# Kernel tuning notes

Hardware: AMD Instinct MI355X
Metric: run time of the kernel (lower is better)

The kernel has to match this reference:

```python
import jax, jax.numpy as jnp
import numpy as np

B, S, D, H = 2, 2048, 1024, 16  # batch, seq, rep_dim, num_heads
DH = D // H
MASK_VALUE = -1e-06  # value passed by MHAttention to masked_softmax (NOT -1e6)


def setup_inputs() -> dict:
    key = jax.random.key(0)
    ks = jax.random.split(key, 16)
    def xavier(k, shape):
        fan_in, fan_out = shape[0], shape[1]
        limit = float(np.sqrt(6.0 / (fan_in + fan_out)))
        return jax.random.uniform(k, shape, jnp.float32, -limit, limit)
    return {
        "queries": jax.random.normal(ks[0], (B, S, D), jnp.float32),
        "keys": jax.random.normal(ks[1], (B, S, D), jnp.float32),
        "values": jax.random.normal(ks[2], (B, S, D), jnp.float32),
        "thresholds": jax.random.randint(ks[3], (B,), 1, S + 1, jnp.int32),
        # Linear params stored as (in, out) so y = x @ W + b
        "Wq": xavier(ks[4], (D, D)), "bq": jnp.zeros((D,), jnp.float32),
        "Wk": xavier(ks[5], (D, D)), "bk": jnp.zeros((D,), jnp.float32),
        "Wv": xavier(ks[6], (D, D)), "bv": jnp.zeros((D,), jnp.float32),
        "W": xavier(ks[7], (DH, DH)),  # learnable bilinear attention matrix
        "Wo": xavier(ks[8], (D, D)), "bo": jnp.zeros((D,), jnp.float32),
    }


def reference(queries, keys, values, thresholds, Wq, bq, Wk, bk, Wv, bv, W, Wo, bo):
    def split_heads(x):  # (B,S,D) -> (B,H,S,DH)
        return x.reshape(B, S, H, DH).transpose(0, 2, 1, 3)

    Q = split_heads(queries @ Wq + bq)
    K = split_heads(keys @ Wk + bk)
    V = split_heads(values @ Wv + bv)

    # bilinear scores: (Q @ W) @ K^T, no 1/sqrt(d) scaling in original
    scores = jnp.einsum("bhqd,bhkd->bhqk", Q @ W, K)
    # mask key positions >= threshold[b] with MASK_VALUE before softmax
    keep = jnp.arange(S)[None, None, None, :] < thresholds[:, None, None, None]
    scores = jnp.where(keep, scores, MASK_VALUE)
    attn = jax.nn.softmax(scores, axis=-1)

    out = jnp.einsum("bhqk,bhkd->bhqd", attn, V)
    out = out.transpose(0, 2, 1, 3).reshape(B, S, D)  # merge heads
    return out @ Wo + bo
```

## Files before the change

kernel.cpp:

```cpp
#include <hip/hip_runtime.h>
#include <hip/hip_bf16.h>

#define D_MODEL 1024
#define NHEADS  16
#define DH      64
#define SEQ     2048
#define BATCH   2

#define LOG2E 1.4426950408889634f
#define MASKB2 (-1e-6f * LOG2E)
#define DEFER_THR 11.5456f
#define NEG_INF (-__builtin_inff())

typedef __attribute__((ext_vector_type(8))) short short8;
typedef __attribute__((ext_vector_type(4))) short short4v;
typedef __attribute__((ext_vector_type(4))) float f32x4;

#define AS1C(p) ((const __attribute__((address_space(1))) void*)(p))
#define AS3(p)  ((__attribute__((address_space(3))) void*)(p))

union PB { short4v s4; unsigned int u[2]; };
union VU { short8 s8; short4v h[2]; };

static __device__ __forceinline__ float fexp2(float x) {
    return __builtin_amdgcn_exp2f(x);
}

static __device__ __forceinline__ unsigned int pk2(float lo, float hi) {
    __hip_bfloat16 a = __float2bfloat16(lo), b = __float2bfloat16(hi);
    unsigned short au = *(unsigned short*)&a, bu = *(unsigned short*)&b;
    return (unsigned int)au | ((unsigned int)bu << 16);
}

__global__ __launch_bounds__(256) void prep_all_kernel(
    const float* __restrict__ Wq, const float* __restrict__ bq, const float* __restrict__ W,
    __hip_bfloat16* __restrict__ WqT, float* __restrict__ bq2,
    const float* __restrict__ Wk, const float* __restrict__ Wv, const float* __restrict__ Wo,
    __hip_bfloat16* __restrict__ WkT, __hip_bfloat16* __restrict__ WvT,
    __hip_bfloat16* __restrict__ WoT,
    const float* __restrict__ q, const float* __restrict__ k, const float* __restrict__ v,
    __hip_bfloat16* __restrict__ oq, __hip_bfloat16* __restrict__ ok,
    __hip_bfloat16* __restrict__ ov) {
    const int blk = blockIdx.x;
    const int t = threadIdx.x;

    if (blk < 1056) {
        const int c0 = (blk & 31) * 32;
        const int yy = blk >> 5;
        const int h = c0 >> 6, j0 = c0 & 63;
        if (yy == 32) {
            if (t < 32) {
                int col = c0 + t, j = col & 63;
                float s = 0.f;
#pragma unroll
                for (int d = 0; d < DH; ++d) s += bq[h * DH + d] * W[d * DH + j];
                bq2[col] = s * LOG2E;
            }
            return;
        }
        const int r0 = yy * 32;
        __shared__ float sWq[32][68];
        __shared__ float sW[64][36];
        __shared__ float sOut[32][33];
        {
            int lr = t >> 3, lc8 = (t & 7) * 8;
            const float* src = Wq + (size_t)(r0 + lr) * D_MODEL + h * DH + lc8;
            *(float4*)&sWq[lr][lc8]     = *(const float4*)(src);
            *(float4*)&sWq[lr][lc8 + 4] = *(const float4*)(src + 4);
            int d = t >> 2, c8 = (t & 3) * 8;
            const float* wsrc = W + (size_t)d * DH + j0 + c8;
            *(float4*)&sW[d][c8]     = *(const float4*)(wsrc);
            *(float4*)&sW[d][c8 + 4] = *(const float4*)(wsrc + 4);
        }
        __syncthreads();
        {
            int col_loc = t & 31, rq = t >> 5;
            float acc0 = 0.f, acc1 = 0.f, acc2 = 0.f, acc3 = 0.f;
#pragma unroll
            for (int d = 0; d < 64; ++d) {
                float wv = sW[d][col_loc];
                acc0 += sWq[rq * 4 + 0][d] * wv;
                acc1 += sWq[rq * 4 + 1][d] * wv;
                acc2 += sWq[rq * 4 + 2][d] * wv;
                acc3 += sWq[rq * 4 + 3][d] * wv;
            }
            sOut[col_loc][rq * 4 + 0] = acc0 * LOG2E;
            sOut[col_loc][rq * 4 + 1] = acc1 * LOG2E;
            sOut[col_loc][rq * 4 + 2] = acc2 * LOG2E;
            sOut[col_loc][rq * 4 + 3] = acc3 * LOG2E;
        }
        __syncthreads();
        {
            int orow = t >> 3, oc4 = (t & 7) * 4;
            __hip_bfloat16 o4[4];
#pragma unroll
            for (int i = 0; i < 4; ++i) o4[i] = __float2bfloat16(sOut[orow][oc4 + i]);
            *(short4*)(WqT + (size_t)(c0 + orow) * D_MODEL + r0 + oc4) = *(short4*)o4;
        }
    } else if (blk < 4128) {
        __shared__ float sT[32][33];
        int r = blk - 1056;
        int z = r >> 10; r &= 1023;
        const float* Win = (z == 0) ? Wk : (z == 1) ? Wv : Wo;
        __hip_bfloat16* Wt = (z == 0) ? WkT : (z == 1) ? WvT : WoT;
        int n0 = (r & 31) * 32, k0 = (r >> 5) * 32;
        int tx = t & 31, ty = t >> 5;
#pragma unroll
        for (int i = 0; i < 4; ++i)
            sT[ty + i * 8][tx] = Win[(size_t)(k0 + ty + i * 8) * D_MODEL + n0 + tx];
        __syncthreads();
#pragma unroll
        for (int i = 0; i < 4; ++i)
            Wt[(size_t)(n0 + ty + i * 8) * D_MODEL + k0 + tx] =
                __float2bfloat16(sT[tx][ty + i * 8]);
    } else {
        int idx = blk - 4128;
        int z = idx >> 11;
        int i = (idx & 2047) * 256 + t;
        const float* in = (z == 0) ? q : (z == 1) ? k : v;
        __hip_bfloat16* out = (z == 0) ? oq : (z == 1) ? ok : ov;
        float4 a = *(const float4*)(in + (size_t)i * 8);
        float4 b = *(const float4*)(in + (size_t)i * 8 + 4);
        __hip_bfloat16 o[8];
        o[0] = __float2bfloat16(a.x); o[1] = __float2bfloat16(a.y);
        o[2] = __float2bfloat16(a.z); o[3] = __float2bfloat16(a.w);
        o[4] = __float2bfloat16(b.x); o[5] = __float2bfloat16(b.y);
        o[6] = __float2bfloat16(b.z); o[7] = __float2bfloat16(b.w);
        *(short8*)(out + (size_t)i * 8) = *(short8*)o;
    }
}

#define GEMM_CORE(A_, BT_)                                                                  \
    __shared__ __hip_bfloat16 sA[2][128 * 32];                                              \
    __shared__ __hip_bfloat16 sB[2][128 * 32];                                              \
    const int t = threadIdx.x;                                                              \
    const int lane = t & 63, w = t >> 6;                                                    \
    const int g = lane >> 4, li = lane & 15;                                                \
    const int lin = blockIdx.y * 8 + blockIdx.x;                                            \
    const int ob = (lin & 7) * 32 + (lin >> 3);                                             \
    const int r0 = (ob >> 3) * 128, c0 = (ob & 7) * 128;                                    \
    const int wr = (w >> 1) * 64, wc = (w & 1) * 64;                                        \
    f32x4 acc[4][4] = {};                                                                   \
    auto stage = [&](int bb, int k0) {                                                      \
        _Pragma("unroll")                                                                   \
        for (int i = 0; i < 2; ++i) {                                                       \
            int o = (i * 4 + w) * 1024 + lane * 16;                                         \
            int row = o >> 6, ce = (o & 63) >> 1;                                           \
            __builtin_amdgcn_global_load_lds(AS1C(A_ + (size_t)(r0 + row) * 1024 + k0 + ce),\
                                             AS3((char*)sA[bb] + (i * 4 + w) * 1024), 16, 0, 0); \
            __builtin_amdgcn_global_load_lds(AS1C(BT_ + (size_t)(c0 + row) * 1024 + k0 + ce),\
                                             AS3((char*)sB[bb] + (i * 4 + w) * 1024), 16, 0, 0); \
        }                                                                                   \
    };                                                                                      \
    stage(0, 0);                                                                            \
    asm volatile("s_waitcnt vmcnt(0)" ::: "memory");                                        \
    __syncthreads();                                                                        \
    int cur = 0;                                                                            \
    for (int k0 = 0; k0 < 1024; k0 += 32) {                                                 \
        if (k0 + 32 < 1024) stage(cur ^ 1, k0 + 32);                                        \
        short8 af[4], bf[4];                                                                \
        _Pragma("unroll")                                                                   \
        for (int m = 0; m < 4; ++m)                                                         \
            af[m] = *(const short8*)(sA[cur] + (wr + m * 16 + li) * 32 + g * 8);            \
        _Pragma("unroll")                                                                   \
        for (int n = 0; n < 4; ++n)                                                         \
            bf[n] = *(const short8*)(sB[cur] + (wc + n * 16 + li) * 32 + g * 8);            \
        _Pragma("unroll")                                                                   \
        for (int m = 0; m < 4; ++m)                                                         \
            _Pragma("unroll")                                                               \
            for (int n = 0; n < 4; ++n)                                                     \
                acc[m][n] = __builtin_amdgcn_mfma_f32_16x16x32_bf16(af[m], bf[n], acc[m][n], 0, 0, 0); \
        asm volatile("s_waitcnt vmcnt(0)" ::: "memory");                                    \
        __syncthreads();                                                                    \
        cur ^= 1;                                                                           \
    }

__global__ __launch_bounds__(256) void gemm_qkv_kernel(
    const __hip_bfloat16* __restrict__ Xq, const __hip_bfloat16* __restrict__ Xk,
    const __hip_bfloat16* __restrict__ Xv,
    const __hip_bfloat16* __restrict__ WqT, const __hip_bfloat16* __restrict__ WkT,
    const __hip_bfloat16* __restrict__ WvT,
    const float* __restrict__ bq2, const float* __restrict__ bk, const float* __restrict__ bv,
    __hip_bfloat16* __restrict__ Qp, __hip_bfloat16* __restrict__ Kp,
    __hip_bfloat16* __restrict__ Vt) {
    const int z = blockIdx.z;
    const __hip_bfloat16* A  = (z == 0) ? Xq  : (z == 1) ? Xk  : Xv;
    const __hip_bfloat16* BT = (z == 0) ? WqT : (z == 1) ? WkT : WvT;
    const float* bias        = (z == 0) ? bq2 : (z == 1) ? bk  : bv;
    __hip_bfloat16* C        = (z == 0) ? Qp  : (z == 1) ? Kp  : Vt;

    GEMM_CORE(A, BT)

#pragma unroll
    for (int m = 0; m < 4; ++m) {
#pragma unroll
        for (int n = 0; n < 4; ++n) {
            int col = c0 + wc + n * 16 + li;
            float bs = bias[col];
            int row0 = r0 + wr + m * 16 + g * 4;
            int h = col >> 6, d = col & 63;
            if (z == 2) {
                int b = row0 >> 11, s0 = row0 & 2047;
                int sp = (s0 & ~127) | (((s0 >> 2) & 3) << 5) | (((s0 >> 4) & 7) << 2);
                __hip_bfloat16 o4[4];
#pragma unroll
                for (int r = 0; r < 4; ++r) o4[r] = __float2bfloat16(acc[m][n][r] + bs);
                *(short4*)(C + (((size_t)(b * NHEADS + h)) * DH + d) * SEQ + sp) = *(short4*)o4;
            } else {
#pragma unroll
                for (int r = 0; r < 4; ++r) {
                    int row = row0 + r;
                    int b = row >> 11, s = row & 2047;
                    C[(((size_t)(b * NHEADS + h)) * SEQ + s) * DH + d] =
                        __float2bfloat16(acc[m][n][r] + bs);
                }
            }
        }
    }
}

__global__ __launch_bounds__(256) void gemm_out_kernel(
    const __hip_bfloat16* __restrict__ A, const __hip_bfloat16* __restrict__ BT,
    const float* __restrict__ bias, float* __restrict__ C) {
    GEMM_CORE(A, BT)
#pragma unroll
    for (int m = 0; m < 4; ++m) {
#pragma unroll
        for (int n = 0; n < 4; ++n) {
            int col = c0 + wc + n * 16 + li;
            float bs = bias[col];
            int row0 = r0 + wr + m * 16 + g * 4;
#pragma unroll
            for (int r = 0; r < 4; ++r)
                C[(size_t)(row0 + r) * D_MODEL + col] = acc[m][n][r] + bs;
        }
    }
}

__global__ __launch_bounds__(256) void vsum_kernel(const __hip_bfloat16* __restrict__ Vt,
                                                   const int* __restrict__ thresholds,
                                                   float* __restrict__ Vsum) {
    int bh = blockIdx.x, b = bh >> 4;
    int thresh = thresholds[b];
    int loop_end = min(SEQ, ((thresh + 127) >> 7) << 7);
    int t = threadIdx.x;
    int dh = t >> 2, sub = t & 3;
    const __hip_bfloat16* row = Vt + ((size_t)bh * DH + dh) * SEQ;
    float s = 0.f;
    for (int s0 = loop_end + sub * 8; s0 < SEQ; s0 += 32) {
        short8 v = *(const short8*)(row + s0);
#pragma unroll
        for (int j = 0; j < 8; ++j) {
            unsigned short us = (unsigned short)v[j];
            s += __bfloat162float(*(__hip_bfloat16*)&us);
        }
    }
    s += __shfl_xor(s, 1);
    s += __shfl_xor(s, 2);
    if (sub == 0) Vsum[bh * DH + dh] = s;
}

__global__ __launch_bounds__(512, 4) void attn_mfma_kernel(
    const __hip_bfloat16* __restrict__ Qp,
    const __hip_bfloat16* __restrict__ Kp,
    const __hip_bfloat16* __restrict__ Vt,
    const int* __restrict__ thresholds,
    const float* __restrict__ Vsum,
    __hip_bfloat16* __restrict__ AO) {
    __shared__ char lds[65536];
    char* sK  = lds;
    char* sVT = lds + 32768;

    const int t = threadIdx.x, lane = t & 63, w = t >> 6;
    const int g = lane >> 4, li = lane & 15;
    const int bh = blockIdx.x, b = bh >> 4, h = bh & 15;
    const int q0 = blockIdx.y * 128;
    const int thresh = thresholds[b];
    const int loop_end = min(SEQ, ((thresh + 127) >> 7) << 7);
    const __hip_bfloat16* Qb = Qp + (size_t)bh * SEQ * DH;
    const __hip_bfloat16* Kb = Kp + (size_t)bh * SEQ * DH;
    const __hip_bfloat16* Vb = Vt + (size_t)bh * DH * SEQ;

    short8 qf[2];
#pragma unroll
    for (int kb = 0; kb < 2; ++kb)
        qf[kb] = *(const short8*)(Qb + (size_t)(q0 + w * 16 + li) * DH + kb * 32 + g * 8);

    f32x4 Oacc[4] = {};
    float mrun = NEG_INF, lpart = 0.f;

    auto stageK = [&](int bb, int kv) {
#pragma unroll
        for (int i = 0; i < 2; ++i) {
            int o = i * 8192 + t * 16;
            int key = o >> 7, slot = (o & 127) >> 4;
            __builtin_amdgcn_global_load_lds(
                AS1C(Kb + (size_t)(kv + key) * DH + ((slot ^ (key & 7)) << 3)),
                AS3(sK + bb * 16384 + i * 8192 + w * 1024), 16, 0, 0);
        }
    };
    auto stageV = [&](int bb, int kv) {
#pragma unroll
        for (int i = 0; i < 2; ++i) {
            int o = i * 8192 + t * 16;
            int dh = o >> 8, slot = (o & 255) >> 4;
            __builtin_amdgcn_global_load_lds(
                AS1C(Vb + (size_t)dh * SEQ + kv + ((slot ^ (dh & 15)) << 3)),
                AS3(sVT + bb * 16384 + i * 8192 + w * 1024), 16, 0, 0);
        }
    };

    stageK(0, 0); stageV(0, 0);
    asm volatile("s_waitcnt vmcnt(0)" ::: "memory");
    __syncthreads();

    int cur = 0;
    for (int kv0 = 0; kv0 < loop_end; kv0 += 128) {
        int nxt = kv0 + 128;
        if (nxt < loop_end) { stageK(cur ^ 1, nxt); stageV(cur ^ 1, nxt); }

        f32x4 S[8] = {};
        __builtin_amdgcn_s_setprio(1);
#pragma unroll
        for (int kb = 0; kb < 2; ++kb) {
            short8 kf[8];
#pragma unroll
            for (int n = 0; n < 8; ++n) {
                int key = 16 * n + li;
                kf[n] = *(const short8*)(sK + cur * 16384 + key * 128 +
                                         (((4 * kb + g) ^ (key & 7)) << 4));
            }
#pragma unroll
            for (int n = 0; n < 8; ++n)
                S[n] = __builtin_amdgcn_mfma_f32_16x16x32_bf16(kf[n], qf[kb], S[n], 0, 0, 0);
        }
        __builtin_amdgcn_s_setprio(0);

        if (kv0 + 128 > thresh) {
            int tr = thresh - kv0 - 4 * g;
#pragma unroll
            for (int n = 0; n < 8; ++n)
#pragma unroll
                for (int rr = 0; rr < 4; ++rr)
                    if (16 * n + rr >= tr) S[n][rr] = MASKB2;
        }

        float mx = S[0][0];
#pragma unroll
        for (int n = 0; n < 8; ++n)
#pragma unroll
            for (int rr = 0; rr < 4; ++rr) mx = fmaxf(mx, S[n][rr]);
        mx = fmaxf(mx, __shfl_xor(mx, 16));
        mx = fmaxf(mx, __shfl_xor(mx, 32));
        float pmax = mx;

        if (__any(pmax > mrun + DEFER_THR)) {
            float mn = fmaxf(mrun, pmax);
            float alpha = fexp2(mrun - mn);
            lpart *= alpha;
#pragma unroll
            for (int n = 0; n < 4; ++n)
#pragma unroll
                for (int rr = 0; rr < 4; ++rr) Oacc[n][rr] *= alpha;
            mrun = mn;
        }

        short4v pb[8];
#pragma unroll
        for (int n = 0; n < 8; ++n) {
#pragma unroll
            for (int rr = 0; rr < 4; ++rr) {
                float p = fexp2(S[n][rr] - mrun);
                S[n][rr] = p;
                lpart += p;
            }
            PB u;
            u.u[0] = pk2(S[n][0], S[n][1]);
            u.u[1] = pk2(S[n][2], S[n][3]);
            pb[n] = u.s4;
        }

        __builtin_amdgcn_s_setprio(1);
#pragma unroll
        for (int u = 0; u < 4; ++u) {
            int slot = 4 * g + u;
#pragma unroll
            for (int n = 0; n < 4; ++n) {
                int dh = 16 * n + li;
                VU vu;
                vu.s8 = *(const short8*)(sVT + cur * 16384 + dh * 256 +
                                         ((slot ^ (dh & 15)) << 4));
                Oacc[n] = __builtin_amdgcn_mfma_f32_16x16x16bf16_1k(vu.h[0], pb[2 * u],
                                                                    Oacc[n], 0, 0, 0);
                Oacc[n] = __builtin_amdgcn_mfma_f32_16x16x16bf16_1k(vu.h[1], pb[2 * u + 1],
                                                                    Oacc[n], 0, 0, 0);
            }
        }
        __builtin_amdgcn_s_setprio(0);

        asm volatile("s_waitcnt vmcnt(0)" ::: "memory");
        __syncthreads();
        cur ^= 1;
    }

    float lrun = lpart;
    lrun += __shfl_xor(lrun, 16);
    lrun += __shfl_xor(lrun, 32);

    int nmask = SEQ - loop_end;
    if (nmask > 0) {
        const float* vs = Vsum + bh * DH;
        f32x4 vsf[4];
#pragma unroll
        for (int n = 0; n < 4; ++n) vsf[n] = *(const f32x4*)(vs + 16 * n + 4 * g);
        float pu = fexp2(MASKB2 - mrun);
        lrun += (float)nmask * pu;
#pragma unroll
        for (int n = 0; n < 4; ++n)
#pragma unroll
            for (int rr = 0; rr < 4; ++rr) Oacc[n][rr] += pu * vsf[n][rr];
    }

    float linv = 1.0f / lrun;
    int q = q0 + w * 16 + li;
#pragma unroll
    for (int n = 0; n < 4; ++n) {
        __hip_bfloat16 o4[4];
#pragma unroll
        for (int rr = 0; rr < 4; ++rr) o4[rr] = __float2bfloat16(Oacc[n][rr] * linv);
        *(short4*)(AO + (size_t)(b * SEQ + q) * D_MODEL + h * DH + 16 * n + 4 * g) =
            *(short4*)o4;
    }
}

extern "C" void kernel_launch(void* const* d_in, const int* in_sizes, int n_in,
                              void* d_out, int out_size, void* d_ws, size_t ws_size,
                              hipStream_t stream) {
    const float* queries    = (const float*)d_in[0];
    const float* keys       = (const float*)d_in[1];
    const float* values     = (const float*)d_in[2];
    const int*   thresholds = (const int*)d_in[3];
    const float* Wq = (const float*)d_in[4];
    const float* bq = (const float*)d_in[5];
    const float* Wk = (const float*)d_in[6];
    const float* bk = (const float*)d_in[7];
    const float* Wv = (const float*)d_in[8];
    const float* bv = (const float*)d_in[9];
    const float* W  = (const float*)d_in[10];
    const float* Wo = (const float*)d_in[11];
    const float* bo = (const float*)d_in[12];
    float* out = (float*)d_out;

    char* wsb = (char*)d_ws;
    float* bq2  = (float*)wsb;
    float* Vsum = (float*)(wsb + 4096);
    __hip_bfloat16* XqB = (__hip_bfloat16*)(wsb + 16384);
    __hip_bfloat16* XkB = XqB + (1 << 22);
    __hip_bfloat16* XvB = XkB + (1 << 22);
    __hip_bfloat16* WqT = XvB + (1 << 22);
    __hip_bfloat16* WkT = WqT + (1 << 20);
    __hip_bfloat16* WvT = WkT + (1 << 20);
    __hip_bfloat16* WoT = WvT + (1 << 20);
    __hip_bfloat16* QpB = WoT + (1 << 20);
    __hip_bfloat16* KpB = QpB + (1 << 22);
    __hip_bfloat16* VtB = KpB + (1 << 22);
    __hip_bfloat16* AOB = XqB;

    prep_all_kernel<<<10272, 256, 0, stream>>>(Wq, bq, W, WqT, bq2,
                                               Wk, Wv, Wo, WkT, WvT, WoT,
                                               queries, keys, values, XqB, XkB, XvB);

    gemm_qkv_kernel<<<dim3(8, 32, 3), 256, 0, stream>>>(XqB, XkB, XvB, WqT, WkT, WvT,
                                                        bq2, bk, bv, QpB, KpB, VtB);
    vsum_kernel<<<32, 256, 0, stream>>>(VtB, thresholds, Vsum);

    attn_mfma_kernel<<<dim3(32, 16), 512, 0, stream>>>(QpB, KpB, VtB, thresholds, Vsum, AOB);

    gemm_out_kernel<<<dim3(8, 32), 256, 0, stream>>>(AOB, WoT, bo, out);
}
```

Measured before the change: 146.1 us.

## Give each attention wave two query tiles to reuse K/V LDS fragments

The attention kernel now runs 4 waves of 256 threads instead of 8, and each wave handles 32 query rows as two 16-row tiles. Each K and V fragment read from LDS feeds two MFMAs, which halves LDS read traffic per FLOP. The K/V staging loops are reworked so 256 threads still fill the same 128-key tiles. The cost is roughly doubled accumulator and score register use per thread and fewer waves to hide latency, with launch bounds relaxed to 2 blocks per CU.

```diff
diff --git a/kernel.cpp b/kernel.cpp
--- a/kernel.cpp
+++ b/kernel.cpp
@@ -260,7 +260,7 @@
     if (sub == 0) Vsum[bh * DH + dh] = s;
 }
 
-__global__ __launch_bounds__(512, 4) void attn_mfma_kernel(
+__global__ __launch_bounds__(256, 2) void attn_mfma_kernel(
     const __hip_bfloat16* __restrict__ Qp,
     const __hip_bfloat16* __restrict__ Kp,
     const __hip_bfloat16* __restrict__ Vt,
@@ -281,32 +281,36 @@
     const __hip_bfloat16* Kb = Kp + (size_t)bh * SEQ * DH;
     const __hip_bfloat16* Vb = Vt + (size_t)bh * DH * SEQ;
 
-    short8 qf[2];
-#pragma unroll
-    for (int kb = 0; kb < 2; ++kb)
-        qf[kb] = *(const short8*)(Qb + (size_t)(q0 + w * 16 + li) * DH + kb * 32 + g * 8);
-
-    f32x4 Oacc[4] = {};
-    float mrun = NEG_INF, lpart = 0.f;
+    short8 qf[2][2];
+#pragma unroll
+    for (int mq = 0; mq < 2; ++mq)
+#pragma unroll
+        for (int kb = 0; kb < 2; ++kb)
+            qf[mq][kb] = *(const short8*)(Qb + (size_t)(q0 + w * 32 + mq * 16 + li) * DH +
+                                          kb * 32 + g * 8);
+
+    f32x4 Oacc[2][4] = {};
+    float mrun[2] = {NEG_INF, NEG_INF};
+    float lpart[2] = {0.f, 0.f};
 
     auto stageK = [&](int bb, int kv) {
 #pragma unroll
-        for (int i = 0; i < 2; ++i) {
-            int o = i * 8192 + t * 16;
+        for (int i = 0; i < 4; ++i) {
+            int o = i * 4096 + w * 1024 + lane * 16;
             int key = o >> 7, slot = (o & 127) >> 4;
             __builtin_amdgcn_global_load_lds(
                 AS1C(Kb + (size_t)(kv + key) * DH + ((slot ^ (key & 7)) << 3)),
-                AS3(sK + bb * 16384 + i * 8192 + w * 1024), 16, 0, 0);
+                AS3(sK + bb * 16384 + i * 4096 + w * 1024), 16, 0, 0);
         }
     };
     auto stageV = [&](int bb, int kv) {
 #pragma unroll
-        for (int i = 0; i < 2; ++i) {
-            int o = i * 8192 + t * 16;
+        for (int i = 0; i < 4; ++i) {
+            int o = i * 4096 + w * 1024 + lane * 16;
             int dh = o >> 8, slot = (o & 255) >> 4;
             __builtin_amdgcn_global_load_lds(
                 AS1C(Vb + (size_t)dh * SEQ + kv + ((slot ^ (dh & 15)) << 3)),
-                AS3(sVT + bb * 16384 + i * 8192 + w * 1024), 16, 0, 0);
+                AS3(sVT + bb * 16384 + i * 4096 + w * 1024), 16, 0, 0);
         }
     };
 
@@ -319,7 +323,7 @@
         int nxt = kv0 + 128;
         if (nxt < loop_end) { stageK(cur ^ 1, nxt); stageV(cur ^ 1, nxt); }
 
-        f32x4 S[8] = {};
+        f32x4 S[2][8] = {};
         __builtin_amdgcn_s_setprio(1);
 #pragma unroll
         for (int kb = 0; kb < 2; ++kb) {
@@ -331,8 +335,10 @@
                                          (((4 * kb + g) ^ (key & 7)) << 4));
             }
 #pragma unroll
-            for (int n = 0; n < 8; ++n)
-                S[n] = __builtin_amdgcn_mfma_f32_16x16x32_bf16(kf[n], qf[kb], S[n], 0, 0, 0);
+            for (int n = 0; n < 8; ++n) {
+                S[0][n] = __builtin_amdgcn_mfma_f32_16x16x32_bf16(kf[n], qf[0][kb], S[0][n], 0, 0, 0);
+                S[1][n] = __builtin_amdgcn_mfma_f32_16x16x32_bf16(kf[n], qf[1][kb], S[1][n], 0, 0, 0);
+            }
         }
         __builtin_amdgcn_s_setprio(0);
 
@@ -342,43 +348,53 @@
             for (int n = 0; n < 8; ++n)
 #pragma unroll
                 for (int rr = 0; rr < 4; ++rr)
-                    if (16 * n + rr >= tr) S[n][rr] = MASKB2;
-        }
-
-        float mx = S[0][0];
-#pragma unroll
-        for (int n = 0; n < 8; ++n)
-#pragma unroll
-            for (int rr = 0; rr < 4; ++rr) mx = fmaxf(mx, S[n][rr]);
-        mx = fmaxf(mx, __shfl_xor(mx, 16));
-        mx = fmaxf(mx, __shfl_xor(mx, 32));
-        float pmax = mx;
-
-        if (__any(pmax > mrun + DEFER_THR)) {
-            float mn = fmaxf(mrun, pmax);
-            float alpha = fexp2(mrun - mn);
-            lpart *= alpha;
-#pragma unroll
-            for (int n = 0; n < 4; ++n)
-#pragma unroll
-                for (int rr = 0; rr < 4; ++rr) Oacc[n][rr] *= alpha;
-            mrun = mn;
-        }
-
-        short4v pb[8];
-#pragma unroll
-        for (int n = 0; n < 8; ++n) {
-#pragma unroll
-            for (int rr = 0; rr < 4; ++rr) {
-                float p = fexp2(S[n][rr] - mrun);
-                S[n][rr] = p;
-                lpart += p;
-            }
-            PB u;
-            u.u[0] = pk2(S[n][0], S[n][1]);
-            u.u[1] = pk2(S[n][2], S[n][3]);
-            pb[n] = u.s4;
-        }
+                    if (16 * n + rr >= tr) { S[0][n][rr] = MASKB2; S[1][n][rr] = MASKB2; }
+        }
+
+        float pmax[2];
+#pragma unroll
+        for (int mq = 0; mq < 2; ++mq) {
+            float mx = S[mq][0][0];
+#pragma unroll
+            for (int n = 0; n < 8; ++n)
+#pragma unroll
+                for (int rr = 0; rr < 4; ++rr) mx = fmaxf(mx, S[mq][n][rr]);
+            mx = fmaxf(mx, __shfl_xor(mx, 16));
+            mx = fmaxf(mx, __shfl_xor(mx, 32));
+            pmax[mq] = mx;
+        }
+
+        bool need = (pmax[0] > mrun[0] + DEFER_THR) || (pmax[1] > mrun[1] + DEFER_THR);
+        if (__any(need)) {
+#pragma unroll
+            for (int mq = 0; mq < 2; ++mq) {
+                float mn = fmaxf(mrun[mq], pmax[mq]);
+                float alpha = fexp2(mrun[mq] - mn);
+                lpart[mq] *= alpha;
+#pragma unroll
+                for (int n = 0; n < 4; ++n)
+#pragma unroll
+                    for (int rr = 0; rr < 4; ++rr) Oacc[mq][n][rr] *= alpha;
+                mrun[mq] = mn;
+            }
+        }
+
+        short4v pb[2][8];
+#pragma unroll
+        for (int mq = 0; mq < 2; ++mq)
+#pragma unroll
+            for (int n = 0; n < 8; ++n) {
+#pragma unroll
+                for (int rr = 0; rr < 4; ++rr) {
+                    float p = fexp2(S[mq][n][rr] - mrun[mq]);
+                    S[mq][n][rr] = p;
+                    lpart[mq] += p;
+                }
+                PB u;
+                u.u[0] = pk2(S[mq][n][0], S[mq][n][1]);
+                u.u[1] = pk2(S[mq][n][2], S[mq][n][3]);
+                pb[mq][n] = u.s4;
+            }
 
         __builtin_amdgcn_s_setprio(1);
 #pragma unroll
@@ -390,10 +406,14 @@
                 VU vu;
                 vu.s8 = *(const short8*)(sVT + cur * 16384 + dh * 256 +
                                          ((slot ^ (dh & 15)) << 4));
-                Oacc[n] = __builtin_amdgcn_mfma_f32_16x16x16bf16_1k(vu.h[0], pb[2 * u],
-                                                                    Oacc[n], 0, 0, 0);
-                Oacc[n] = __builtin_amdgcn_mfma_f32_16x16x16bf16_1k(vu.h[1], pb[2 * u + 1],
-                                                                    Oacc[n], 0, 0, 0);
+                Oacc[0][n] = __builtin_amdgcn_mfma_f32_16x16x16bf16_1k(vu.h[0], pb[0][2 * u],
+                                                                       Oacc[0][n], 0, 0, 0);
+                Oacc[0][n] = __builtin_amdgcn_mfma_f32_16x16x16bf16_1k(vu.h[1], pb[0][2 * u + 1],
+                                                                       Oacc[0][n], 0, 0, 0);
+                Oacc[1][n] = __builtin_amdgcn_mfma_f32_16x16x16bf16_1k(vu.h[0], pb[1][2 * u],
+                                                                       Oacc[1][n], 0, 0, 0);
+                Oacc[1][n] = __builtin_amdgcn_mfma_f32_16x16x16bf16_1k(vu.h[1], pb[1][2 * u + 1],
+                                                                       Oacc[1][n], 0, 0, 0);
             }
         }
         __builtin_amdgcn_s_setprio(0);
@@ -403,9 +423,14 @@
         cur ^= 1;
     }
 
-    float lrun = lpart;
-    lrun += __shfl_xor(lrun, 16);
-    lrun += __shfl_xor(lrun, 32);
+    float lrun[2];
+#pragma unroll
+    for (int mq = 0; mq < 2; ++mq) {
+        float l = lpart[mq];
+        l += __shfl_xor(l, 16);
+        l += __shfl_xor(l, 32);
+        lrun[mq] = l;
+    }
 
     int nmask = SEQ - loop_end;
     if (nmask > 0) {
@@ -413,23 +438,29 @@
         f32x4 vsf[4];
 #pragma unroll
         for (int n = 0; n < 4; ++n) vsf[n] = *(const f32x4*)(vs + 16 * n + 4 * g);
-        float pu = fexp2(MASKB2 - mrun);
-        lrun += (float)nmask * pu;
-#pragma unroll
-        for (int n = 0; n < 4; ++n)
-#pragma unroll
-            for (int rr = 0; rr < 4; ++rr) Oacc[n][rr] += pu * vsf[n][rr];
-    }
-
-    float linv = 1.0f / lrun;
-    int q = q0 + w * 16 + li;
-#pragma unroll
-    for (int n = 0; n < 4; ++n) {
-        __hip_bfloat16 o4[4];
-#pragma unroll
-        for (int rr = 0; rr < 4; ++rr) o4[rr] = __float2bfloat16(Oacc[n][rr] * linv);
-        *(short4*)(AO + (size_t)(b * SEQ + q) * D_MODEL + h * DH + 16 * n + 4 * g) =
-            *(short4*)o4;
+#pragma unroll
+        for (int mq = 0; mq < 2; ++mq) {
+            float pu = fexp2(MASKB2 - mrun[mq]);
+            lrun[mq] += (float)nmask * pu;
+#pragma unroll
+            for (int n = 0; n < 4; ++n)
+#pragma unroll
+                for (int rr = 0; rr < 4; ++rr) Oacc[mq][n][rr] += pu * vsf[n][rr];
+        }
+    }
+
+#pragma unroll
+    for (int mq = 0; mq < 2; ++mq) {
+        float linv = 1.0f / lrun[mq];
+        int q = q0 + w * 32 + mq * 16 + li;
+#pragma unroll
+        for (int n = 0; n < 4; ++n) {
+            __hip_bfloat16 o4[4];
+#pragma unroll
+            for (int rr = 0; rr < 4; ++rr) o4[rr] = __float2bfloat16(Oacc[mq][n][rr] * linv);
+            *(short4*)(AO + (size_t)(b * SEQ + q) * D_MODEL + h * DH + 16 * n + 4 * g) =
+                *(short4*)o4;
+        }
     }
 }
 
@@ -474,7 +505,7 @@
                                                         bq2, bk, bv, QpB, KpB, VtB);
     vsum_kernel<<<32, 256, 0, stream>>>(VtB, thresholds, Vsum);
 
-    attn_mfma_kernel<<<dim3(32, 16), 512, 0, stream>>>(QpB, KpB, VtB, thresholds, Vsum, AOB);
+    attn_mfma_kernel<<<dim3(32, 16), 256, 0, stream>>>(QpB, KpB, VtB, thresholds, Vsum, AOB);
 
     gemm_out_kernel<<<dim3(8, 32), 256, 0, stream>>>(AOB, WoT, bo, out);
 }
```

New measurement: 151.3 us. 3.6% more time.
